# Kernel optimization log

Measured on AMD Instinct MI355X. Metric: run time of the kernel, lower is better.

## Reference

```python
import jax, jax.numpy as jnp
import numpy as np

N_NODES = 50000
N_EDGES = 800000
D_IN, D1, D2, D_OUT = 128, 150, 100, 64


def setup_inputs() -> dict:
    key = jax.random.key(0)
    ks = jax.random.split(key, 10)
    x = jax.random.normal(ks[0], (N_NODES, D_IN), dtype=jnp.float32)
    src = jax.random.randint(ks[1], (N_EDGES,), 0, N_NODES, dtype=jnp.int32)
    dst = jax.random.randint(ks[2], (N_EDGES,), 0, N_NODES, dtype=jnp.int32)
    s1 = 1.0 / np.sqrt(D_IN)
    s2 = 1.0 / np.sqrt(D1)
    s3 = 1.0 / np.sqrt(D2)
    W1 = jax.random.uniform(ks[3], (D_IN, D1), jnp.float32, -s1, s1)
    b1 = jnp.zeros((D1,), jnp.float32)
    Wn = jax.random.uniform(ks[4], (D1, D2), jnp.float32, -s2, s2)
    Ws = jax.random.uniform(ks[5], (D1, D2), jnp.float32, -s2, s2)
    b2 = jnp.zeros((D2,), jnp.float32)
    W3 = jax.random.uniform(ks[6], (D2, D_OUT), jnp.float32, -s3, s3)
    b3 = jnp.zeros((D_OUT,), jnp.float32)
    return {"x": x, "src": src, "dst": dst, "W1": W1, "b1": b1,
            "Wn": Wn, "Ws": Ws, "b2": b2, "W3": W3, "b3": b3}


def _degrees(src, dst, n):
    ones = jnp.ones(src.shape[0], jnp.float32)
    deg_out = jax.ops.segment_sum(ones, src, num_segments=n)
    deg_in = jax.ops.segment_sum(ones, dst, num_segments=n)
    return deg_out, deg_in


def reference(x, src, dst, W1, b1, Wn, Ws, b2, W3, b3):
    n = x.shape[0]
    deg_out, deg_in = _degrees(src, dst, n)
    norm_out = jax.lax.rsqrt(jnp.maximum(deg_out, 1.0))  # [N]
    norm_in = jax.lax.rsqrt(jnp.maximum(deg_in, 1.0))    # [N]

    # --- GraphConv (norm='both'): D_in^{-1/2} A D_out^{-1/2} X W + b ---
    h = x * norm_out[:, None]                                   # [N, D_IN]
    agg = jax.ops.segment_sum(h[src], dst, num_segments=n)      # [N, D_IN]
    h = (agg * norm_in[:, None]) @ W1 + b1                      # [N, D1]
    h = jax.nn.elu(h)

    # --- SAGEConv (mean): fc_self(h) + fc_neigh(mean_neighbors(h)) + b ---
    neigh_sum = jax.ops.segment_sum(h[src], dst, num_segments=n)  # [N, D1]
    neigh = neigh_sum / jnp.maximum(deg_in, 1.0)[:, None]
    h = h @ Ws + neigh @ Wn + b2                                  # [N, D2]
    h = jax.nn.elu(h)

    # --- Dense + ELU ---
    out = jax.nn.elu(h @ W3 + b3)                                 # [N, D_OUT]
    return out
```

## Files before the change

kernel.cpp:

```cpp
#include <hip/hip_runtime.h>
#include <math.h>

#define N_NODES 50000
#define N_EDGES 800000
#define D_IN 128
#define D1 150
#define LD1 152
#define D2 100
#define LDP 128
#define D_OUT 64
#define SLOT 64
#define HBLK 64
#define HBIN 12500

#define LDS_K 40

using short8 = __attribute__((ext_vector_type(8))) short;
using f32x4  = __attribute__((ext_vector_type(4))) float;

__device__ __forceinline__ float elu(float v) { return v > 0.0f ? v : expm1f(v); }

__device__ __forceinline__ void split_bf16(float a, unsigned short& h, unsigned short& l) {
    unsigned int bits = __float_as_uint(a);
    unsigned int hb = (bits + 0x8000u) >> 16;
    h = (unsigned short)hb;
    float r = a - __uint_as_float(hb << 16);
    l = (unsigned short)((__float_as_uint(r) + 0x8000u) >> 16);
}

__device__ __forceinline__ void split_store16(unsigned short* hrow, unsigned short* lrow,
                                              const float* vv) {
    short8 h0, h1v, l0, l1v;
#pragma unroll
    for (int i = 0; i < 8; ++i) {
        unsigned short hh, ll;
        split_bf16(vv[i], hh, ll);
        h0[i] = (short)hh; l0[i] = (short)ll;
    }
#pragma unroll
    for (int i = 0; i < 8; ++i) {
        unsigned short hh, ll;
        split_bf16(vv[8 + i], hh, ll);
        h1v[i] = (short)hh; l1v[i] = (short)ll;
    }
    *(short8*)(hrow) = h0;
    *(short8*)(hrow + 8) = h1v;
    *(short8*)(lrow) = l0;
    *(short8*)(lrow + 8) = l1v;
}

__global__ __launch_bounds__(256) void hist_kernel(const int* __restrict__ src,
                                                   unsigned int* __restrict__ partial) {
    __shared__ unsigned int bins[HBIN];
    int tid = threadIdx.x, b = blockIdx.x;
    for (int i = tid; i < HBIN; i += 256) bins[i] = 0u;
    __syncthreads();
    int e0 = b * (N_EDGES / HBLK);
    int e1 = e0 + (N_EDGES / HBLK);
    for (int e = e0 + tid; e < e1; e += 256) {
        int s = src[e];
        atomicAdd(&bins[s >> 2], 1u << ((s & 3) * 8));
    }
    __syncthreads();
    unsigned int* outp = partial + (size_t)b * HBIN;
    for (int i = tid; i < HBIN; i += 256) outp[i] = bins[i];
}

__global__ __launch_bounds__(256) void norm_kernel(const unsigned int* __restrict__ partial,
                                                   float* __restrict__ norm_out) {
    int i = blockIdx.x * blockDim.x + threadIdx.x;
    if (i >= HBIN) return;
    unsigned int acc = 0;
#pragma unroll
    for (int h = 0; h < HBLK; ++h) acc += partial[(size_t)h * HBIN + i];
#pragma unroll
    for (int j = 0; j < 4; ++j) {
        unsigned int dg = (acc >> (j * 8)) & 0xFF;
        norm_out[i * 4 + j] = rsqrtf(fmaxf((float)dg, 1.0f));
    }
}

__global__ void fill_kernel(const int* __restrict__ src, const int* __restrict__ dst,
                            int* __restrict__ cursor, unsigned short* __restrict__ slots) {
    int e = blockIdx.x * blockDim.x + threadIdx.x;
    if (e < N_EDGES) {
        int d = dst[e], s = src[e];
        int pos = atomicAdd(&cursor[d], 1);
        if (pos < SLOT) slots[d * SLOT + pos] = (unsigned short)s;
    }
}

__global__ __launch_bounds__(256) void gather_x(const float* __restrict__ x,
                                                const float* __restrict__ norm_out,
                                                const int* __restrict__ deg_in,
                                                const unsigned short* __restrict__ slots,
                                                float* __restrict__ agg) {
    int wave = threadIdx.x >> 6;
    int lane = threadIdx.x & 63;
    int half = lane >> 5;
    int c = lane & 31;
    int n = blockIdx.x * 4 + wave;
    if (n >= N_NODES) return;
    int beg = n * SLOT;
    int dg = deg_in[n]; if (dg > SLOT) dg = SLOT;
    int end = beg + dg;
    float4 acc = {0.0f, 0.0f, 0.0f, 0.0f};
    int e = beg + half;
    for (; e + 2 < end; e += 4) {
        int s0 = slots[e];
        int s1 = slots[e + 2];
        float w0 = norm_out[s0], w1 = norm_out[s1];
        float4 v0 = ((const float4*)(x + (size_t)s0 * D_IN))[c];
        float4 v1 = ((const float4*)(x + (size_t)s1 * D_IN))[c];
        acc.x += v0.x * w0 + v1.x * w1;
        acc.y += v0.y * w0 + v1.y * w1;
        acc.z += v0.z * w0 + v1.z * w1;
        acc.w += v0.w * w0 + v1.w * w1;
    }
    if (e < end) {
        int s = slots[e];
        float w = norm_out[s];
        float4 v = ((const float4*)(x + (size_t)s * D_IN))[c];
        acc.x += v.x * w; acc.y += v.y * w; acc.z += v.z * w; acc.w += v.w * w;
    }
    acc.x += __shfl_xor(acc.x, 32);
    acc.y += __shfl_xor(acc.y, 32);
    acc.z += __shfl_xor(acc.z, 32);
    acc.w += __shfl_xor(acc.w, 32);
    if (half == 0) ((float4*)(agg + (size_t)n * D_IN))[c] = acc;
}

__global__ __launch_bounds__(256) void gather_p(const float* __restrict__ p,
                                                const int* __restrict__ deg_in,
                                                const unsigned short* __restrict__ slots,
                                                float* __restrict__ ns) {
    int wave = threadIdx.x >> 6;
    int lane = threadIdx.x & 63;
    int half = lane >> 5;
    int c = lane & 31;
    bool cv = c < D2 / 4;
    int n = blockIdx.x * 4 + wave;
    if (n >= N_NODES) return;
    int beg = n * SLOT;
    int dg = deg_in[n]; if (dg > SLOT) dg = SLOT;
    int end = beg + dg;
    float4 acc = {0.0f, 0.0f, 0.0f, 0.0f};
    if (cv) {
        int e = beg + half;
        for (; e + 2 < end; e += 4) {
            int s0 = slots[e];
            int s1 = slots[e + 2];
            float4 v0 = ((const float4*)(p + (size_t)s0 * LDP))[c];
            float4 v1 = ((const float4*)(p + (size_t)s1 * LDP))[c];
            acc.x += v0.x + v1.x;
            acc.y += v0.y + v1.y;
            acc.z += v0.z + v1.z;
            acc.w += v0.w + v1.w;
        }
        if (e < end) {
            int s = slots[e];
            float4 v = ((const float4*)(p + (size_t)s * LDP))[c];
            acc.x += v.x; acc.y += v.y; acc.z += v.z; acc.w += v.w;
        }
    }
    acc.x += __shfl_xor(acc.x, 32);
    acc.y += __shfl_xor(acc.y, 32);
    acc.z += __shfl_xor(acc.z, 32);
    acc.w += __shfl_xor(acc.w, 32);
    if (half == 0 && cv) ((float4*)(ns + (size_t)n * LDP))[c] = acc;
}


template <int K, int KP, int NW, int LDA, int PRE, int EPI, int LDC>
__global__ __launch_bounds__(256, 2)
void gemm_mfma(const float* __restrict__ A, const float* __restrict__ W,
               const float* __restrict__ nsrc, const int* __restrict__ deg,
               const float* __restrict__ bstage, const float* __restrict__ bepi,
               float* __restrict__ C) {
    __shared__ __align__(16) unsigned short AsH[128][LDS_K];
    __shared__ __align__(16) unsigned short AsL[128][LDS_K];
    __shared__ __align__(16) unsigned short BsH[64][LDS_K];
    __shared__ __align__(16) unsigned short BsL[64][LDS_K];

    const int tid = threadIdx.x;
    const int m0 = blockIdx.x * 128;
    const int n0 = blockIdx.y * 64;

    const int arow = tid >> 1;
    const int af = (tid & 1) * 16;
    const int grow = m0 + arow;
    const int bn = tid & 63;
    const int bkg = tid >> 6;
    const int bcol = n0 + bn;
    const int wid = tid >> 6;
    const int lane = tid & 63;
    const int wm = (wid >> 1) * 64;
    const int wn = (wid & 1) * 32;
    const int fr = lane & 15;
    const int fg = lane >> 4;

    float invd = 1.0f;
    if (PRE) {
        int dv = (grow < N_NODES) ? deg[grow] : 1;
        invd = 1.0f / fmaxf((float)dv, 1.0f);
    }

    f32x4 acc[4][2];
#pragma unroll
    for (int i = 0; i < 4; ++i)
#pragma unroll
        for (int j = 0; j < 2; ++j) acc[i][j] = {0.0f, 0.0f, 0.0f, 0.0f};

    for (int k0 = 0; k0 < KP; k0 += 32) {
        __syncthreads();
        if (grow < N_NODES && k0 + 32 <= K) {
            const float* ap = A + (size_t)grow * LDA + k0 + af;
            float vv[16];
            if (!PRE) {
                float4 v0 = *(const float4*)(ap + 0);
                float4 v1 = *(const float4*)(ap + 4);
                float4 v2 = *(const float4*)(ap + 8);
                float4 v3 = *(const float4*)(ap + 12);
                vv[0] = v0.x;  vv[1] = v0.y;  vv[2] = v0.z;  vv[3] = v0.w;
                vv[4] = v1.x;  vv[5] = v1.y;  vv[6] = v1.z;  vv[7] = v1.w;
                vv[8] = v2.x;  vv[9] = v2.y;  vv[10] = v2.z; vv[11] = v2.w;
                vv[12] = v3.x; vv[13] = v3.y; vv[14] = v3.z; vv[15] = v3.w;
            } else {
                const float* np = nsrc + (size_t)grow * LDP + k0 + af;
#pragma unroll
                for (int h = 0; h < 4; ++h) {
                    float4 a = *(const float4*)(ap + h * 4);
                    float4 nv = *(const float4*)(np + h * 4);
                    int kb = k0 + af + h * 4;
                    vv[h * 4 + 0] = elu(a.x + bstage[kb + 0] + nv.x * invd);
                    vv[h * 4 + 1] = elu(a.y + bstage[kb + 1] + nv.y * invd);
                    vv[h * 4 + 2] = elu(a.z + bstage[kb + 2] + nv.z * invd);
                    vv[h * 4 + 3] = elu(a.w + bstage[kb + 3] + nv.w * invd);
                }
            }
            split_store16(&AsH[arow][af], &AsL[arow][af], vv);
        } else {
#pragma unroll
            for (int i = 0; i < 16; ++i) {
                int k = k0 + af + i;
                float v = 0.0f;
                if (grow < N_NODES && k < K) {
                    if (!PRE) v = A[(size_t)grow * LDA + k];
                    else
                        v = elu(A[(size_t)grow * LDA + k] + bstage[k] +
                                nsrc[(size_t)grow * LDP + k] * invd);
                }
                unsigned short hh, ll;
                split_bf16(v, hh, ll);
                AsH[arow][af + i] = hh;
                AsL[arow][af + i] = ll;
            }
        }
        {
            short8 hh8, ll8;
#pragma unroll
            for (int kk = 0; kk < 8; ++kk) {
                int k = k0 + bkg * 8 + kk;
                float w = (k < K && bcol < NW) ? W[(size_t)k * NW + bcol] : 0.0f;
                unsigned short hh, ll;
                split_bf16(w, hh, ll);
                hh8[kk] = (short)hh; ll8[kk] = (short)ll;
            }
            *(short8*)&BsH[bn][bkg * 8] = hh8;
            *(short8*)&BsL[bn][bkg * 8] = ll8;
        }
        __syncthreads();
        short8 ah[4], al[4], bh[2], bl[2];
#pragma unroll
        for (int fi = 0; fi < 4; ++fi) {
            ah[fi] = *(const short8*)&AsH[wm + fi * 16 + fr][fg * 8];
            al[fi] = *(const short8*)&AsL[wm + fi * 16 + fr][fg * 8];
        }
#pragma unroll
        for (int fj = 0; fj < 2; ++fj) {
            bh[fj] = *(const short8*)&BsH[wn + fj * 16 + fr][fg * 8];
            bl[fj] = *(const short8*)&BsL[wn + fj * 16 + fr][fg * 8];
        }
#pragma unroll
        for (int fi = 0; fi < 4; ++fi)
#pragma unroll
            for (int fj = 0; fj < 2; ++fj) {
                acc[fi][fj] = __builtin_amdgcn_mfma_f32_16x16x32_bf16(ah[fi], bh[fj], acc[fi][fj], 0, 0, 0);
                acc[fi][fj] = __builtin_amdgcn_mfma_f32_16x16x32_bf16(al[fi], bh[fj], acc[fi][fj], 0, 0, 0);
                acc[fi][fj] = __builtin_amdgcn_mfma_f32_16x16x32_bf16(ah[fi], bl[fj], acc[fi][fj], 0, 0, 0);
            }
    }

#pragma unroll
    for (int fi = 0; fi < 4; ++fi) {
#pragma unroll
        for (int r = 0; r < 4; ++r) {
            int row = m0 + wm + fi * 16 + fg * 4 + r;
            if (row >= N_NODES) continue;
            float rmul = 1.0f;
            if (EPI == 1) rmul = rsqrtf(fmaxf((float)deg[row], 1.0f));
#pragma unroll
            for (int fj = 0; fj < 2; ++fj) {
                int col = n0 + wn + fj * 16 + fr;
                if (col >= LDC) continue;
                float v = 0.0f;
                if (col < NW) {
                    v = acc[fi][fj][r];
                    if (EPI == 1) v = elu(v * rmul + bepi[col]);
                    else if (EPI == 3) v = elu(v + bepi[col]);
                }
                C[(size_t)row * LDC + col] = v;
            }
        }
    }
}

__global__ __launch_bounds__(256, 2)
void gemm_dual_mfma(const float* __restrict__ h1, const float* __restrict__ Wn,
                    const float* __restrict__ Ws, float* __restrict__ p,
                    float* __restrict__ h2pre) {
    __shared__ __align__(16) unsigned short AsH[128][LDS_K];
    __shared__ __align__(16) unsigned short AsL[128][LDS_K];
    __shared__ __align__(16) unsigned short BsH[64][LDS_K];
    __shared__ __align__(16) unsigned short BsL[64][LDS_K];

    const int tid = threadIdx.x;
    const int m0 = blockIdx.x * 128;
    const int yy = blockIdx.y;
    const int n0 = (yy & 1) * 64;
    const float* W = (yy < 2) ? Wn : Ws;

    const int arow = tid >> 1;
    const int af = (tid & 1) * 16;
    const int grow = m0 + arow;
    const int bn = tid & 63;
    const int bkg = tid >> 6;
    const int bcol = n0 + bn;
    const int wid = tid >> 6;
    const int lane = tid & 63;
    const int wm = (wid >> 1) * 64;
    const int wn = (wid & 1) * 32;
    const int fr = lane & 15;
    const int fg = lane >> 4;

    f32x4 acc[4][2];
#pragma unroll
    for (int i = 0; i < 4; ++i)
#pragma unroll
        for (int j = 0; j < 2; ++j) acc[i][j] = {0.0f, 0.0f, 0.0f, 0.0f};

    for (int k0 = 0; k0 < 160; k0 += 32) {
        __syncthreads();
        if (grow < N_NODES && k0 + 32 <= D1) {
            const float* ap = h1 + (size_t)grow * LD1 + k0 + af;
            float4 v0 = *(const float4*)(ap + 0);
            float4 v1 = *(const float4*)(ap + 4);
            float4 v2 = *(const float4*)(ap + 8);
            float4 v3 = *(const float4*)(ap + 12);
            float vv[16] = {v0.x, v0.y, v0.z, v0.w, v1.x, v1.y, v1.z, v1.w,
                            v2.x, v2.y, v2.z, v2.w, v3.x, v3.y, v3.z, v3.w};
            split_store16(&AsH[arow][af], &AsL[arow][af], vv);
        } else {
#pragma unroll
            for (int i = 0; i < 16; ++i) {
                int k = k0 + af + i;
                float v = (grow < N_NODES && k < D1) ? h1[(size_t)grow * LD1 + k] : 0.0f;
                unsigned short hh, ll;
                split_bf16(v, hh, ll);
                AsH[arow][af + i] = hh;
                AsL[arow][af + i] = ll;
            }
        }
        {
            short8 hh8, ll8;
#pragma unroll
            for (int kk = 0; kk < 8; ++kk) {
                int k = k0 + bkg * 8 + kk;
                float w = (k < D1 && bcol < D2) ? W[(size_t)k * D2 + bcol] : 0.0f;
                unsigned short hh, ll;
                split_bf16(w, hh, ll);
                hh8[kk] = (short)hh; ll8[kk] = (short)ll;
            }
            *(short8*)&BsH[bn][bkg * 8] = hh8;
            *(short8*)&BsL[bn][bkg * 8] = ll8;
        }
        __syncthreads();
        short8 ah[4], al[4], bh[2], bl[2];
#pragma unroll
        for (int fi = 0; fi < 4; ++fi) {
            ah[fi] = *(const short8*)&AsH[wm + fi * 16 + fr][fg * 8];
            al[fi] = *(const short8*)&AsL[wm + fi * 16 + fr][fg * 8];
        }
#pragma unroll
        for (int fj = 0; fj < 2; ++fj) {
            bh[fj] = *(const short8*)&BsH[wn + fj * 16 + fr][fg * 8];
            bl[fj] = *(const short8*)&BsL[wn + fj * 16 + fr][fg * 8];
        }
#pragma unroll
        for (int fi = 0; fi < 4; ++fi)
#pragma unroll
            for (int fj = 0; fj < 2; ++fj) {
                acc[fi][fj] = __builtin_amdgcn_mfma_f32_16x16x32_bf16(ah[fi], bh[fj], acc[fi][fj], 0, 0, 0);
                acc[fi][fj] = __builtin_amdgcn_mfma_f32_16x16x32_bf16(al[fi], bh[fj], acc[fi][fj], 0, 0, 0);
                acc[fi][fj] = __builtin_amdgcn_mfma_f32_16x16x32_bf16(ah[fi], bl[fj], acc[fi][fj], 0, 0, 0);
            }
    }

#pragma unroll
    for (int fi = 0; fi < 4; ++fi) {
#pragma unroll
        for (int r = 0; r < 4; ++r) {
            int row = m0 + wm + fi * 16 + fg * 4 + r;
            if (row >= N_NODES) continue;
#pragma unroll
            for (int fj = 0; fj < 2; ++fj) {
                int col = n0 + wn + fj * 16 + fr;
                float v = acc[fi][fj][r];
                if (yy < 2) {
                    p[(size_t)row * LDP + col] = (col < D2) ? v : 0.0f;
                } else {
                    if (col < D2) h2pre[(size_t)row * D2 + col] = v;
                }
            }
        }
    }
}

extern "C" void kernel_launch(void* const* d_in, const int* in_sizes, int n_in,
                              void* d_out, int out_size, void* d_ws, size_t ws_size,
                              hipStream_t stream) {
    const float* x  = (const float*)d_in[0];
    const int* src  = (const int*)d_in[1];
    const int* dst  = (const int*)d_in[2];
    const float* W1 = (const float*)d_in[3];
    const float* b1 = (const float*)d_in[4];
    const float* Wn = (const float*)d_in[5];
    const float* Ws = (const float*)d_in[6];
    const float* b2 = (const float*)d_in[7];
    const float* W3 = (const float*)d_in[8];
    const float* b3 = (const float*)d_in[9];
    float* out = (float*)d_out;

    char* wsb = (char*)d_ws;
    unsigned int* partial = (unsigned int*)wsb;
    int*   cursor     = (int*)wsb + 800000;
    float* norm_out   = (float*)wsb + 850000;
    unsigned short* slots = (unsigned short*)((float*)wsb + 900000);
    float* agg        = (float*)wsb + 2500000;
    float* h1         = (float*)wsb + 8900000;
    float* h2pre      = (float*)wsb + 16500000;
    float* p          = agg;
    float* ns         = h1;
    int*   deg_in     = cursor;

    hipMemsetAsync(cursor, 0, N_NODES * sizeof(int), stream);

    hist_kernel<<<HBLK, 256, 0, stream>>>(src, partial);
    fill_kernel<<<(N_EDGES + 255) / 256, 256, 0, stream>>>(src, dst, cursor, slots);
    norm_kernel<<<(HBIN + 255) / 256, 256, 0, stream>>>(partial, norm_out);
    gather_x<<<(N_NODES + 3) / 4, 256, 0, stream>>>(x, norm_out, deg_in, slots, agg);

    const int MB = (N_NODES + 127) / 128;
    gemm_mfma<128, 128, 150, 128, 0, 1, LD1><<<dim3(MB, 3), 256, 0, stream>>>(
        agg, W1, nullptr, deg_in, nullptr, b1, h1);
    gemm_dual_mfma<<<dim3(MB, 4), 256, 0, stream>>>(h1, Wn, Ws, p, h2pre);
    gather_p<<<(N_NODES + 3) / 4, 256, 0, stream>>>(p, deg_in, slots, ns);
    gemm_mfma<100, 128, 64, 100, 1, 3, D_OUT><<<dim3(MB, 1), 256, 0, stream>>>(
        h2pre, W3, ns, deg_in, b2, b3, out);
}
```

Measured before the change: 368.0 us.

## Prefetch GEMM tiles into registers and remap blocks for XCD-grouped N-tiles

The GEMM kernels now load the next K-tile from global memory into registers while the current tile is converted and multiplied from LDS, a software double-buffering scheme. The 2D grid becomes a 1D grid in which blocks sharing the same row tile but different column tiles are spaced by 8, which likely aims to place them on the same XCD so A rows are reused in its L2. Launch bounds rise to 3 waves-per-EU for non-PRE kernels, and B fragments are loaded per column group to cut register pressure. The extra prefetch registers may offset the occupancy gain, and the early-return padding blocks add a little waste.

```diff
diff --git a/kernel.cpp b/kernel.cpp
--- a/kernel.cpp
+++ b/kernel.cpp
@@ -171,21 +171,30 @@
 }
 
 
-template <int K, int KP, int NW, int LDA, int PRE, int EPI, int LDC>
-__global__ __launch_bounds__(256, 2)
+template <int K, int KP, int NW, int LDA, int PRE, int EPI, int LDC, int GROUP>
+__global__ __launch_bounds__(256, PRE ? 2 : 3)
 void gemm_mfma(const float* __restrict__ A, const float* __restrict__ W,
                const float* __restrict__ nsrc, const int* __restrict__ deg,
                const float* __restrict__ bstage, const float* __restrict__ bepi,
                float* __restrict__ C) {
+    constexpr int NSTEP = KP / 32;
+    constexpr int MBLK = (N_NODES + 127) / 128;
     __shared__ __align__(16) unsigned short AsH[128][LDS_K];
     __shared__ __align__(16) unsigned short AsL[128][LDS_K];
     __shared__ __align__(16) unsigned short BsH[64][LDS_K];
     __shared__ __align__(16) unsigned short BsL[64][LDS_K];
 
+    const int b = blockIdx.x;
+    const int c = b & 7;
+    const int sIdx = b >> 3;
+    const int jj = sIdx / GROUP;
+    const int yy = sIdx - jj * GROUP;
+    const int xb = c + 8 * jj;
+    if (xb >= MBLK) return;
+    const int m0 = xb * 128;
+    const int n0 = yy * 64;
+
     const int tid = threadIdx.x;
-    const int m0 = blockIdx.x * 128;
-    const int n0 = blockIdx.y * 64;
-
     const int arow = tid >> 1;
     const int af = (tid & 1) * 16;
     const int grow = m0 + arow;
@@ -211,66 +220,86 @@
 #pragma unroll
         for (int j = 0; j < 2; ++j) acc[i][j] = {0.0f, 0.0f, 0.0f, 0.0f};
 
-    for (int k0 = 0; k0 < KP; k0 += 32) {
-        __syncthreads();
+    auto load_a = [&](int k0, float* vA, float* vN) {
         if (grow < N_NODES && k0 + 32 <= K) {
             const float* ap = A + (size_t)grow * LDA + k0 + af;
-            float vv[16];
-            if (!PRE) {
-                float4 v0 = *(const float4*)(ap + 0);
-                float4 v1 = *(const float4*)(ap + 4);
-                float4 v2 = *(const float4*)(ap + 8);
-                float4 v3 = *(const float4*)(ap + 12);
-                vv[0] = v0.x;  vv[1] = v0.y;  vv[2] = v0.z;  vv[3] = v0.w;
-                vv[4] = v1.x;  vv[5] = v1.y;  vv[6] = v1.z;  vv[7] = v1.w;
-                vv[8] = v2.x;  vv[9] = v2.y;  vv[10] = v2.z; vv[11] = v2.w;
-                vv[12] = v3.x; vv[13] = v3.y; vv[14] = v3.z; vv[15] = v3.w;
-            } else {
+#pragma unroll
+            for (int h = 0; h < 4; ++h) {
+                float4 v = *(const float4*)(ap + h * 4);
+                vA[h * 4 + 0] = v.x; vA[h * 4 + 1] = v.y;
+                vA[h * 4 + 2] = v.z; vA[h * 4 + 3] = v.w;
+            }
+            if (PRE) {
                 const float* np = nsrc + (size_t)grow * LDP + k0 + af;
 #pragma unroll
                 for (int h = 0; h < 4; ++h) {
-                    float4 a = *(const float4*)(ap + h * 4);
-                    float4 nv = *(const float4*)(np + h * 4);
-                    int kb = k0 + af + h * 4;
-                    vv[h * 4 + 0] = elu(a.x + bstage[kb + 0] + nv.x * invd);
-                    vv[h * 4 + 1] = elu(a.y + bstage[kb + 1] + nv.y * invd);
-                    vv[h * 4 + 2] = elu(a.z + bstage[kb + 2] + nv.z * invd);
-                    vv[h * 4 + 3] = elu(a.w + bstage[kb + 3] + nv.w * invd);
+                    float4 v = *(const float4*)(np + h * 4);
+                    vN[h * 4 + 0] = v.x; vN[h * 4 + 1] = v.y;
+                    vN[h * 4 + 2] = v.z; vN[h * 4 + 3] = v.w;
                 }
             }
-            split_store16(&AsH[arow][af], &AsL[arow][af], vv);
+        } else {
+#pragma unroll
+            for (int i = 0; i < 16; ++i) {
+                int k = k0 + af + i;
+                bool ok = (grow < N_NODES && k < K);
+                vA[i] = ok ? A[(size_t)grow * LDA + k] : 0.0f;
+                if (PRE) vN[i] = ok ? nsrc[(size_t)grow * LDP + k] : 0.0f;
+            }
+        }
+    };
+    auto load_b = [&](int k0, float* vB) {
+#pragma unroll
+        for (int kk = 0; kk < 8; ++kk) {
+            int k = k0 + bkg * 8 + kk;
+            vB[kk] = (k < K && bcol < NW) ? W[(size_t)k * NW + bcol] : 0.0f;
+        }
+    };
+    auto stage = [&](int k0, const float* vA, const float* vN, const float* vB) {
+        float tv[16];
+        if (!PRE) {
+#pragma unroll
+            for (int i = 0; i < 16; ++i) tv[i] = vA[i];
+        } else if (grow < N_NODES && k0 + 32 <= K) {
+#pragma unroll
+            for (int i = 0; i < 16; ++i)
+                tv[i] = elu(vA[i] + bstage[k0 + af + i] + vN[i] * invd);
         } else {
 #pragma unroll
             for (int i = 0; i < 16; ++i) {
                 int k = k0 + af + i;
                 float v = 0.0f;
-                if (grow < N_NODES && k < K) {
-                    if (!PRE) v = A[(size_t)grow * LDA + k];
-                    else
-                        v = elu(A[(size_t)grow * LDA + k] + bstage[k] +
-                                nsrc[(size_t)grow * LDP + k] * invd);
-                }
-                unsigned short hh, ll;
-                split_bf16(v, hh, ll);
-                AsH[arow][af + i] = hh;
-                AsL[arow][af + i] = ll;
-            }
-        }
-        {
-            short8 hh8, ll8;
-#pragma unroll
-            for (int kk = 0; kk < 8; ++kk) {
-                int k = k0 + bkg * 8 + kk;
-                float w = (k < K && bcol < NW) ? W[(size_t)k * NW + bcol] : 0.0f;
-                unsigned short hh, ll;
-                split_bf16(w, hh, ll);
-                hh8[kk] = (short)hh; ll8[kk] = (short)ll;
-            }
-            *(short8*)&BsH[bn][bkg * 8] = hh8;
-            *(short8*)&BsL[bn][bkg * 8] = ll8;
+                if (grow < N_NODES && k < K) v = elu(vA[i] + bstage[k] + vN[i] * invd);
+                tv[i] = v;
+            }
+        }
+        split_store16(&AsH[arow][af], &AsL[arow][af], tv);
+        short8 hh8, ll8;
+#pragma unroll
+        for (int kk = 0; kk < 8; ++kk) {
+            unsigned short hh, ll;
+            split_bf16(vB[kk], hh, ll);
+            hh8[kk] = (short)hh; ll8[kk] = (short)ll;
+        }
+        *(short8*)&BsH[bn][bkg * 8] = hh8;
+        *(short8*)&BsL[bn][bkg * 8] = ll8;
+    };
+
+    float bufA[2][16], bufN[2][16], bufB[2][8];
+    load_a(0, bufA[0], bufN[0]);
+    load_b(0, bufB[0]);
+
+#pragma unroll
+    for (int t = 0; t < NSTEP; ++t) {
+        const int cur = t & 1, nxt = cur ^ 1;
+        if (t + 1 < NSTEP) {
+            load_a((t + 1) * 32, bufA[nxt], bufN[nxt]);
+            load_b((t + 1) * 32, bufB[nxt]);
         }
         __syncthreads();
-        short8 ah[4], al[4], bh[2], bl[2];
+        stage(t * 32, bufA[cur], bufN[cur], bufB[cur]);
+        __syncthreads();
+        short8 ah[4], al[4];
 #pragma unroll
         for (int fi = 0; fi < 4; ++fi) {
             ah[fi] = *(const short8*)&AsH[wm + fi * 16 + fr][fg * 8];
@@ -278,17 +307,15 @@
         }
 #pragma unroll
         for (int fj = 0; fj < 2; ++fj) {
-            bh[fj] = *(const short8*)&BsH[wn + fj * 16 + fr][fg * 8];
-            bl[fj] = *(const short8*)&BsL[wn + fj * 16 + fr][fg * 8];
-        }
-#pragma unroll
-        for (int fi = 0; fi < 4; ++fi)
-#pragma unroll
-            for (int fj = 0; fj < 2; ++fj) {
-                acc[fi][fj] = __builtin_amdgcn_mfma_f32_16x16x32_bf16(ah[fi], bh[fj], acc[fi][fj], 0, 0, 0);
-                acc[fi][fj] = __builtin_amdgcn_mfma_f32_16x16x32_bf16(al[fi], bh[fj], acc[fi][fj], 0, 0, 0);
-                acc[fi][fj] = __builtin_amdgcn_mfma_f32_16x16x32_bf16(ah[fi], bl[fj], acc[fi][fj], 0, 0, 0);
-            }
+            short8 bh = *(const short8*)&BsH[wn + fj * 16 + fr][fg * 8];
+            short8 bl = *(const short8*)&BsL[wn + fj * 16 + fr][fg * 8];
+#pragma unroll
+            for (int fi = 0; fi < 4; ++fi) {
+                acc[fi][fj] = __builtin_amdgcn_mfma_f32_16x16x32_bf16(ah[fi], bh, acc[fi][fj], 0, 0, 0);
+                acc[fi][fj] = __builtin_amdgcn_mfma_f32_16x16x32_bf16(al[fi], bh, acc[fi][fj], 0, 0, 0);
+                acc[fi][fj] = __builtin_amdgcn_mfma_f32_16x16x32_bf16(ah[fi], bl, acc[fi][fj], 0, 0, 0);
+            }
+        }
     }
 
 #pragma unroll
@@ -315,21 +342,29 @@
     }
 }
 
-__global__ __launch_bounds__(256, 2)
+__global__ __launch_bounds__(256, 3)
 void gemm_dual_mfma(const float* __restrict__ h1, const float* __restrict__ Wn,
                     const float* __restrict__ Ws, float* __restrict__ p,
                     float* __restrict__ h2pre) {
+    constexpr int NSTEP = 5;
+    constexpr int MBLK = (N_NODES + 127) / 128;
     __shared__ __align__(16) unsigned short AsH[128][LDS_K];
     __shared__ __align__(16) unsigned short AsL[128][LDS_K];
     __shared__ __align__(16) unsigned short BsH[64][LDS_K];
     __shared__ __align__(16) unsigned short BsL[64][LDS_K];
 
-    const int tid = threadIdx.x;
-    const int m0 = blockIdx.x * 128;
-    const int yy = blockIdx.y;
+    const int b = blockIdx.x;
+    const int c = b & 7;
+    const int sIdx = b >> 3;
+    const int jj = sIdx >> 2;
+    const int yy = sIdx & 3;
+    const int xb = c + 8 * jj;
+    if (xb >= MBLK) return;
+    const int m0 = xb * 128;
     const int n0 = (yy & 1) * 64;
     const float* W = (yy < 2) ? Wn : Ws;
 
+    const int tid = threadIdx.x;
     const int arow = tid >> 1;
     const int af = (tid & 1) * 16;
     const int grow = m0 + arow;
@@ -349,43 +384,58 @@
 #pragma unroll
         for (int j = 0; j < 2; ++j) acc[i][j] = {0.0f, 0.0f, 0.0f, 0.0f};
 
-    for (int k0 = 0; k0 < 160; k0 += 32) {
-        __syncthreads();
+    auto load_a = [&](int k0, float* vA) {
         if (grow < N_NODES && k0 + 32 <= D1) {
             const float* ap = h1 + (size_t)grow * LD1 + k0 + af;
-            float4 v0 = *(const float4*)(ap + 0);
-            float4 v1 = *(const float4*)(ap + 4);
-            float4 v2 = *(const float4*)(ap + 8);
-            float4 v3 = *(const float4*)(ap + 12);
-            float vv[16] = {v0.x, v0.y, v0.z, v0.w, v1.x, v1.y, v1.z, v1.w,
-                            v2.x, v2.y, v2.z, v2.w, v3.x, v3.y, v3.z, v3.w};
-            split_store16(&AsH[arow][af], &AsL[arow][af], vv);
+#pragma unroll
+            for (int h = 0; h < 4; ++h) {
+                float4 v = *(const float4*)(ap + h * 4);
+                vA[h * 4 + 0] = v.x; vA[h * 4 + 1] = v.y;
+                vA[h * 4 + 2] = v.z; vA[h * 4 + 3] = v.w;
+            }
         } else {
 #pragma unroll
             for (int i = 0; i < 16; ++i) {
                 int k = k0 + af + i;
-                float v = (grow < N_NODES && k < D1) ? h1[(size_t)grow * LD1 + k] : 0.0f;
-                unsigned short hh, ll;
-                split_bf16(v, hh, ll);
-                AsH[arow][af + i] = hh;
-                AsL[arow][af + i] = ll;
-            }
-        }
-        {
-            short8 hh8, ll8;
-#pragma unroll
-            for (int kk = 0; kk < 8; ++kk) {
-                int k = k0 + bkg * 8 + kk;
-                float w = (k < D1 && bcol < D2) ? W[(size_t)k * D2 + bcol] : 0.0f;
-                unsigned short hh, ll;
-                split_bf16(w, hh, ll);
-                hh8[kk] = (short)hh; ll8[kk] = (short)ll;
-            }
-            *(short8*)&BsH[bn][bkg * 8] = hh8;
-            *(short8*)&BsL[bn][bkg * 8] = ll8;
+                vA[i] = (grow < N_NODES && k < D1) ? h1[(size_t)grow * LD1 + k] : 0.0f;
+            }
+        }
+    };
+    auto load_b = [&](int k0, float* vB) {
+#pragma unroll
+        for (int kk = 0; kk < 8; ++kk) {
+            int k = k0 + bkg * 8 + kk;
+            vB[kk] = (k < D1 && bcol < D2) ? W[(size_t)k * D2 + bcol] : 0.0f;
+        }
+    };
+    auto stage = [&](const float* vA, const float* vB) {
+        split_store16(&AsH[arow][af], &AsL[arow][af], vA);
+        short8 hh8, ll8;
+#pragma unroll
+        for (int kk = 0; kk < 8; ++kk) {
+            unsigned short hh, ll;
+            split_bf16(vB[kk], hh, ll);
+            hh8[kk] = (short)hh; ll8[kk] = (short)ll;
+        }
+        *(short8*)&BsH[bn][bkg * 8] = hh8;
+        *(short8*)&BsL[bn][bkg * 8] = ll8;
+    };
+
+    float bufA[2][16], bufB[2][8];
+    load_a(0, bufA[0]);
+    load_b(0, bufB[0]);
+
+#pragma unroll
+    for (int t = 0; t < NSTEP; ++t) {
+        const int cur = t & 1, nxt = cur ^ 1;
+        if (t + 1 < NSTEP) {
+            load_a((t + 1) * 32, bufA[nxt]);
+            load_b((t + 1) * 32, bufB[nxt]);
         }
         __syncthreads();
-        short8 ah[4], al[4], bh[2], bl[2];
+        stage(bufA[cur], bufB[cur]);
+        __syncthreads();
+        short8 ah[4], al[4];
 #pragma unroll
         for (int fi = 0; fi < 4; ++fi) {
             ah[fi] = *(const short8*)&AsH[wm + fi * 16 + fr][fg * 8];
@@ -393,17 +443,15 @@
         }
 #pragma unroll
         for (int fj = 0; fj < 2; ++fj) {
-            bh[fj] = *(const short8*)&BsH[wn + fj * 16 + fr][fg * 8];
-            bl[fj] = *(const short8*)&BsL[wn + fj * 16 + fr][fg * 8];
-        }
-#pragma unroll
-        for (int fi = 0; fi < 4; ++fi)
-#pragma unroll
-            for (int fj = 0; fj < 2; ++fj) {
-                acc[fi][fj] = __builtin_amdgcn_mfma_f32_16x16x32_bf16(ah[fi], bh[fj], acc[fi][fj], 0, 0, 0);
-                acc[fi][fj] = __builtin_amdgcn_mfma_f32_16x16x32_bf16(al[fi], bh[fj], acc[fi][fj], 0, 0, 0);
-                acc[fi][fj] = __builtin_amdgcn_mfma_f32_16x16x32_bf16(ah[fi], bl[fj], acc[fi][fj], 0, 0, 0);
-            }
+            short8 bh = *(const short8*)&BsH[wn + fj * 16 + fr][fg * 8];
+            short8 bl = *(const short8*)&BsL[wn + fj * 16 + fr][fg * 8];
+#pragma unroll
+            for (int fi = 0; fi < 4; ++fi) {
+                acc[fi][fj] = __builtin_amdgcn_mfma_f32_16x16x32_bf16(ah[fi], bh, acc[fi][fj], 0, 0, 0);
+                acc[fi][fj] = __builtin_amdgcn_mfma_f32_16x16x32_bf16(al[fi], bh, acc[fi][fj], 0, 0, 0);
+                acc[fi][fj] = __builtin_amdgcn_mfma_f32_16x16x32_bf16(ah[fi], bl, acc[fi][fj], 0, 0, 0);
+            }
+        }
     }
 
 #pragma unroll
@@ -461,10 +509,11 @@
     gather_x<<<(N_NODES + 3) / 4, 256, 0, stream>>>(x, norm_out, deg_in, slots, agg);
 
     const int MB = (N_NODES + 127) / 128;
-    gemm_mfma<128, 128, 150, 128, 0, 1, LD1><<<dim3(MB, 3), 256, 0, stream>>>(
+    const int XG = (MB + 7) / 8;
+    gemm_mfma<128, 128, 150, 128, 0, 1, LD1, 3><<<XG * 8 * 3, 256, 0, stream>>>(
         agg, W1, nullptr, deg_in, nullptr, b1, h1);
-    gemm_dual_mfma<<<dim3(MB, 4), 256, 0, stream>>>(h1, Wn, Ws, p, h2pre);
+    gemm_dual_mfma<<<XG * 8 * 4, 256, 0, stream>>>(h1, Wn, Ws, p, h2pre);
     gather_p<<<(N_NODES + 3) / 4, 256, 0, stream>>>(p, deg_in, slots, ns);
-    gemm_mfma<100, 128, 64, 100, 1, 3, D_OUT><<<dim3(MB, 1), 256, 0, stream>>>(
+    gemm_mfma<100, 128, 64, 100, 1, 3, D_OUT, 1><<<XG * 8, 256, 0, stream>>>(
         h2pre, W3, ns, deg_in, b2, b3, out);
 }
```

After: 375.9 us. 1.02x slower.
